# Optimization experiments

Hardware: AMD Instinct MI355X
Metric: run time of the kernel (lower is better)

Reference implementation:

```python
import jax, jax.numpy as jnp
import numpy as np

DECAY = 0.7      # membrane decay
THETA = 1.0      # spike threshold
K_WINNERS = 5
GAIN_UP = 1.5
GAIN_DOWN = 0.6

SEQ_LEN = 8192
VOCAB = 128000


def setup_inputs() -> dict:
    key = jax.random.key(0)
    token_seq = jax.random.randint(key, (SEQ_LEN,), 0, VOCAB)  # int token ids
    v0 = jnp.zeros((VOCAB,), jnp.float32)  # initial membrane potentials
    return {"token_seq": token_seq, "v0": v0, "vocab_size": VOCAB}


def reference(token_seq, v0, vocab_size):
    spikes0 = jnp.zeros((vocab_size,), jnp.float32)

    def lif_step(state, token_id):
        v, spikes = state
        t = jnp.clip(token_id, 0, vocab_size - 1).astype(jnp.int32)
        v_new = DECAY * v[t] + 1.0                      # gather + decay + input current
        spiked = v_new >= THETA
        v = v.at[t].set(jnp.where(spiked, v_new - THETA, v_new))  # reset-by-subtraction
        spikes = spikes.at[t].add(spiked.astype(jnp.float32))
        return (v, spikes), None

    (v_final, spikes_final), _ = jax.lax.scan(lif_step, (v0, spikes0), token_seq)

    k = min(K_WINNERS, int(vocab_size))
    _, top_idx = jax.lax.top_k(v_final, k)
    winners = jnp.zeros((vocab_size,), jnp.float32).at[top_idx].set(1.0)
    gains = jnp.where(winners > 0, GAIN_UP,
                      jnp.where(spikes_final > 0, GAIN_DOWN, 1.0))
    return gains
```

## Files before the change

### kernel.cpp

```cpp
#include <hip/hip_runtime.h>
#include <float.h>
#include <limits.h>

#define DECAY 0.7f
#define THETA 1.0f
#define KWIN 5
#define GAIN_UP 1.5f
#define GAIN_DOWN 0.6f

#define NT 256
#define SLICE 1024

__device__ __forceinline__ void lif_replay(float v0, int n, float& v_out, int& spikes_out) {
    float v = v0;
    int s = 0;
    for (int i = 0; i < n; ++i) {
        float vn = __fadd_rn(__fmul_rn(DECAY, v), 1.0f);
        if (vn >= THETA) { v = __fsub_rn(vn, THETA); ++s; }
        else             { v = vn; }
    }
    v_out = v;
    spikes_out = s;
}

__device__ __forceinline__ void better(float& bv, int& bi, float ov, int oi) {
    if (ov > bv || (ov == bv && oi < bi)) { bv = ov; bi = oi; }
}

__global__ void fused_local(const int* __restrict__ tok,
                            const float* __restrict__ v0,
                            int n, int vocab,
                            float* __restrict__ out,
                            float* __restrict__ cand_v,
                            int* __restrict__ cand_i) {
    __shared__ int hist[SLICE];

    const int tid  = threadIdx.x;
    const int bid  = blockIdx.x;
    const int wave = tid >> 6;
    const int lane = tid & 63;
    const int sbase = bid * SLICE;

    #pragma unroll
    for (int k = 0; k < SLICE / NT; ++k) {
        hist[k * NT + tid] = 0;
    }
    __syncthreads();

    int nv4 = n & ~3;
    for (int j = tid * 4; j < nv4; j += NT * 4) {
        int4 t4 = *(const int4*)(tok + j);
        int t; unsigned r;
        t = min(max(t4.x, 0), vocab - 1); r = (unsigned)(t - sbase); if (r < SLICE) atomicAdd(&hist[r], 1);
        t = min(max(t4.y, 0), vocab - 1); r = (unsigned)(t - sbase); if (r < SLICE) atomicAdd(&hist[r], 1);
        t = min(max(t4.z, 0), vocab - 1); r = (unsigned)(t - sbase); if (r < SLICE) atomicAdd(&hist[r], 1);
        t = min(max(t4.w, 0), vocab - 1); r = (unsigned)(t - sbase); if (r < SLICE) atomicAdd(&hist[r], 1);
    }
    for (int j = nv4 + tid; j < n; j += NT) {
        int t = min(max(tok[j], 0), vocab - 1);
        unsigned r = (unsigned)(t - sbase);
        if (r < SLICE) atomicAdd(&hist[r], 1);
    }
    __syncthreads();

    const int wbase = wave * 256;
    float lv[4];
    int   li[4];
    #pragma unroll
    for (int k = 0; k < 4; ++k) {
        int off = wbase + k * 64 + lane;
        int idx = sbase + off;
        float vf = -FLT_MAX;
        int   id = -1;
        if (idx < vocab) {
            int c = hist[off];
            int s;
            lif_replay(v0[idx], c, vf, s);
            out[idx] = (s > 0) ? GAIN_DOWN : 1.0f;
            id = idx;
        }
        lv[k] = vf;
        li[k] = id;
    }

    const int gw = bid * (NT / 64) + wave;
    #pragma unroll
    for (int r = 0; r < KWIN; ++r) {
        float bv = -FLT_MAX;
        int   bi = INT_MAX;
        #pragma unroll
        for (int k = 0; k < 4; ++k) {
            if (li[k] >= 0) better(bv, bi, lv[k], li[k]);
        }
        #pragma unroll
        for (int off = 32; off > 0; off >>= 1) {
            float ov = __shfl_xor(bv, off, 64);
            int   oi = __shfl_xor(bi, off, 64);
            better(bv, bi, ov, oi);
        }
        if (lane == 0) {
            cand_v[gw * KWIN + r] = bv;
            cand_i[gw * KWIN + r] = bi;
        }
        #pragma unroll
        for (int k = 0; k < 4; ++k) {
            if (li[k] == bi) li[k] = -1;
        }
    }
}

#define MAXC 10

__global__ void merge_top5(const float* __restrict__ cand_v,
                           const int* __restrict__ cand_i,
                           int n_cand,
                           float* __restrict__ out) {
    __shared__ unsigned long long swk[4];

    const int tid  = threadIdx.x;
    const int wave = tid >> 6;
    const int lane = tid & 63;

    unsigned long long k0 = 0ULL, k1 = 0ULL, k2 = 0ULL, k3 = 0ULL, k4 = 0ULL;
    unsigned long long k5 = 0ULL, k6 = 0ULL, k7 = 0ULL, k8 = 0ULL, k9 = 0ULL;
    #pragma unroll
    for (int s = 0; s < MAXC; ++s) {
        int j = s * 256 + tid;
        unsigned long long key = 0ULL;
        if (j < n_cand) {
            int ci = cand_i[j];
            if (ci >= 0 && ci != INT_MAX) {
                unsigned b  = __float_as_uint(cand_v[j]);
                unsigned sv = (b & 0x80000000u) ? ~b : (b | 0x80000000u);
                key = ((unsigned long long)sv << 32) | (unsigned)(~(unsigned)ci);
            }
        }
        if (s == 0) k0 = key; else if (s == 1) k1 = key;
        else if (s == 2) k2 = key; else if (s == 3) k3 = key;
        else if (s == 4) k4 = key; else if (s == 5) k5 = key;
        else if (s == 6) k6 = key; else if (s == 7) k7 = key;
        else if (s == 8) k8 = key; else k9 = key;
    }

    unsigned long long thresh = ~0ULL;
    for (int r = 0; r < KWIN; ++r) {
        unsigned long long best = 0ULL;
        if (k0 < thresh && k0 > best) best = k0;
        if (k1 < thresh && k1 > best) best = k1;
        if (k2 < thresh && k2 > best) best = k2;
        if (k3 < thresh && k3 > best) best = k3;
        if (k4 < thresh && k4 > best) best = k4;
        if (k5 < thresh && k5 > best) best = k5;
        if (k6 < thresh && k6 > best) best = k6;
        if (k7 < thresh && k7 > best) best = k7;
        if (k8 < thresh && k8 > best) best = k8;
        if (k9 < thresh && k9 > best) best = k9;

        #pragma unroll
        for (int off = 32; off > 0; off >>= 1) {
            unsigned hi = (unsigned)(best >> 32);
            unsigned lo = (unsigned)(best & 0xFFFFFFFFu);
            unsigned ohi = __shfl_xor(hi, off, 64);
            unsigned olo = __shfl_xor(lo, off, 64);
            unsigned long long ok = ((unsigned long long)ohi << 32) | olo;
            if (ok > best) best = ok;
        }
        if (lane == 0) swk[wave] = best;
        __syncthreads();

        unsigned long long bb = swk[0];
        if (swk[1] > bb) bb = swk[1];
        if (swk[2] > bb) bb = swk[2];
        if (swk[3] > bb) bb = swk[3];
        __syncthreads();

        if (tid == 0 && bb != 0ULL) {
            unsigned inv = (unsigned)(bb & 0xFFFFFFFFu);
            int idx = (int)(~inv);
            out[idx] = GAIN_UP;
        }
        thresh = bb;
    }
}

extern "C" void kernel_launch(void* const* d_in, const int* in_sizes, int n_in,
                              void* d_out, int out_size, void* d_ws, size_t ws_size,
                              hipStream_t stream) {
    const int*   tok = (const int*)d_in[0];
    const float* v0  = (const float*)d_in[1];
    int n     = in_sizes[0];
    int vocab = in_sizes[1];
    float* out = (float*)d_out;

    int nb     = (vocab + SLICE - 1) / SLICE;
    int nwaves = nb * (NT / 64);

    float* cand_v = (float*)d_ws;
    int*   cand_i = (int*)(cand_v + (size_t)nwaves * KWIN);

    fused_local<<<nb, NT, 0, stream>>>(tok, v0, n, vocab, out, cand_v, cand_i);
    merge_top5<<<1, NT, 0, stream>>>(cand_v, cand_i, nwaves * KWIN, out);
}
```

Baseline: 74.78 us.

## Merge into single kernel with per-block full hash histogram and global top-5

```diff
diff --git a/kernel.cpp b/kernel.cpp
--- a/kernel.cpp
+++ b/kernel.cpp
@@ -8,8 +8,15 @@
 #define GAIN_UP 1.5f
 #define GAIN_DOWN 0.6f
 
-#define NT 256
+#define NT 1024
+#define NWAVES (NT / 64)
 #define SLICE 1024
+#define NSLOT 16384
+#define HMASK (NSLOT - 1)
+#define HEMPTY 0xFFFFFFFFu
+#define CBITS 14
+#define CMASK ((1u << CBITS) - 1u)
+#define BWORDS 4096
 
 __device__ __forceinline__ void lif_replay(float v0, int n, float& v_out, int& spikes_out) {
     float v = v0;
@@ -23,143 +30,125 @@
     spikes_out = s;
 }
 
-__device__ __forceinline__ void better(float& bv, int& bi, float ov, int oi) {
-    if (ov > bv || (ov == bv && oi < bi)) { bv = ov; bi = oi; }
+__device__ __forceinline__ unsigned long long mkkey(float v, int idx) {
+    unsigned b  = __float_as_uint(v);
+    unsigned sv = (b & 0x80000000u) ? ~b : (b | 0x80000000u);
+    return ((unsigned long long)sv << 32) | (unsigned)(~(unsigned)idx);
 }
 
-__global__ void fused_local(const int* __restrict__ tok,
-                            const float* __restrict__ v0,
-                            int n, int vocab,
-                            float* __restrict__ out,
-                            float* __restrict__ cand_v,
-                            int* __restrict__ cand_i) {
-    __shared__ int hist[SLICE];
+__global__ __launch_bounds__(NT) void fused_one(const int* __restrict__ tok,
+                                                const float* __restrict__ v0,
+                                                int n, int vocab,
+                                                float* __restrict__ out) {
+    __shared__ unsigned hsl[NSLOT];
+    __shared__ unsigned bmap[BWORDS];
+    __shared__ unsigned long long swk[NWAVES];
 
-    const int tid  = threadIdx.x;
-    const int bid  = blockIdx.x;
-    const int wave = tid >> 6;
-    const int lane = tid & 63;
+    const int tid   = threadIdx.x;
+    const int bid   = blockIdx.x;
+    const int wave  = tid >> 6;
+    const int lane  = tid & 63;
     const int sbase = bid * SLICE;
 
     #pragma unroll
-    for (int k = 0; k < SLICE / NT; ++k) {
-        hist[k * NT + tid] = 0;
-    }
+    for (int k = 0; k < NSLOT / NT; ++k) hsl[k * NT + tid] = HEMPTY;
+    #pragma unroll
+    for (int k = 0; k < BWORDS / NT; ++k) bmap[k * NT + tid] = 0u;
     __syncthreads();
 
+    auto insert_tok = [&](int traw) {
+        int t = min(max(traw, 0), vocab - 1);
+        atomicOr(&bmap[t >> 5], 1u << (t & 31));
+        unsigned h = ((unsigned)t * 2654435761u) >> 18;
+        for (;;) {
+            unsigned cur = hsl[h];
+            if (cur != HEMPTY && (cur >> CBITS) == (unsigned)t) { atomicAdd(&hsl[h], 1u); break; }
+            if (cur == HEMPTY) {
+                unsigned old = atomicCAS(&hsl[h], HEMPTY, ((unsigned)t << CBITS) | 1u);
+                if (old == HEMPTY) break;
+                if ((old >> CBITS) == (unsigned)t) { atomicAdd(&hsl[h], 1u); break; }
+            }
+            h = (h + 1) & HMASK;
+        }
+    };
     int nv4 = n & ~3;
     for (int j = tid * 4; j < nv4; j += NT * 4) {
         int4 t4 = *(const int4*)(tok + j);
-        int t; unsigned r;
-        t = min(max(t4.x, 0), vocab - 1); r = (unsigned)(t - sbase); if (r < SLICE) atomicAdd(&hist[r], 1);
-        t = min(max(t4.y, 0), vocab - 1); r = (unsigned)(t - sbase); if (r < SLICE) atomicAdd(&hist[r], 1);
-        t = min(max(t4.z, 0), vocab - 1); r = (unsigned)(t - sbase); if (r < SLICE) atomicAdd(&hist[r], 1);
-        t = min(max(t4.w, 0), vocab - 1); r = (unsigned)(t - sbase); if (r < SLICE) atomicAdd(&hist[r], 1);
+        insert_tok(t4.x); insert_tok(t4.y); insert_tok(t4.z); insert_tok(t4.w);
     }
-    for (int j = nv4 + tid; j < n; j += NT) {
-        int t = min(max(tok[j], 0), vocab - 1);
-        unsigned r = (unsigned)(t - sbase);
-        if (r < SLICE) atomicAdd(&hist[r], 1);
-    }
+    for (int j = nv4 + tid; j < n; j += NT) insert_tok(tok[j]);
     __syncthreads();
 
-    const int wbase = wave * 256;
-    float lv[4];
-    int   li[4];
-    #pragma unroll
-    for (int k = 0; k < 4; ++k) {
-        int off = wbase + k * 64 + lane;
-        int idx = sbase + off;
-        float vf = -FLT_MAX;
-        int   id = -1;
-        if (idx < vocab) {
-            int c = hist[off];
-            int s;
-            lif_replay(v0[idx], c, vf, s);
-            out[idx] = (s > 0) ? GAIN_DOWN : 1.0f;
-            id = idx;
+    auto lookup_cnt = [&](int idx) -> int {
+        unsigned h = ((unsigned)idx * 2654435761u) >> 18;
+        for (;;) {
+            unsigned cur = hsl[h];
+            if (cur == HEMPTY) return 0;
+            if ((cur >> CBITS) == (unsigned)idx) return (int)(cur & CMASK);
+            h = (h + 1) & HMASK;
         }
-        lv[k] = vf;
-        li[k] = id;
+    };
+
+    unsigned long long k0 = 0ULL, k1 = 0ULL, k2 = 0ULL, k3 = 0ULL, k4 = 0ULL;
+
+    auto consider = [&](float vf, int idx) {
+        unsigned long long key = mkkey(vf, idx);
+        if (key > k4) {
+            if      (key > k0) { k4 = k3; k3 = k2; k2 = k1; k1 = k0; k0 = key; }
+            else if (key > k1) { k4 = k3; k3 = k2; k2 = k1; k1 = key; }
+            else if (key > k2) { k4 = k3; k3 = k2; k2 = key; }
+            else if (key > k3) { k4 = k3; k3 = key; }
+            else               { k4 = key; }
+        }
+    };
+
+    for (int base = tid * 4; base < vocab; base += NT * 4) {
+        if (base + 3 < vocab) {
+            float4 v4 = *(const float4*)(v0 + base);
+            unsigned bw = bmap[base >> 5];
+            unsigned sh = (unsigned)(base & 31);
+            float g0, g1, g2, g3;
+            float vf; int s;
+
+            if ((bw >> (sh + 0)) & 1u) { lif_replay(v4.x, lookup_cnt(base + 0), vf, s); } else { vf = v4.x; s = 0; }
+            g0 = (s > 0) ? GAIN_DOWN : 1.0f; consider(vf, base + 0);
+            if ((bw >> (sh + 1)) & 1u) { lif_replay(v4.y, lookup_cnt(base + 1), vf, s); } else { vf = v4.y; s = 0; }
+            g1 = (s > 0) ? GAIN_DOWN : 1.0f; consider(vf, base + 1);
+            if ((bw >> (sh + 2)) & 1u) { lif_replay(v4.z, lookup_cnt(base + 2), vf, s); } else { vf = v4.z; s = 0; }
+            g2 = (s > 0) ? GAIN_DOWN : 1.0f; consider(vf, base + 2);
+            if ((bw >> (sh + 3)) & 1u) { lif_replay(v4.w, lookup_cnt(base + 3), vf, s); } else { vf = v4.w; s = 0; }
+            g3 = (s > 0) ? GAIN_DOWN : 1.0f; consider(vf, base + 3);
+
+            if ((unsigned)(base - sbase) < SLICE) {
+                *(float4*)(out + base) = make_float4(g0, g1, g2, g3);
+            }
+        } else {
+            for (int idx = base; idx < vocab; ++idx) {
+                float v = v0[idx];
+                float vf; int s;
+                if ((bmap[idx >> 5] >> (idx & 31)) & 1u) { lif_replay(v, lookup_cnt(idx), vf, s); }
+                else { vf = v; s = 0; }
+                if ((unsigned)(idx - sbase) < SLICE) out[idx] = (s > 0) ? GAIN_DOWN : 1.0f;
+                consider(vf, idx);
+            }
+        }
     }
 
-    const int gw = bid * (NT / 64) + wave;
-    #pragma unroll
-    for (int r = 0; r < KWIN; ++r) {
-        float bv = -FLT_MAX;
-        int   bi = INT_MAX;
-        #pragma unroll
-        for (int k = 0; k < 4; ++k) {
-            if (li[k] >= 0) better(bv, bi, lv[k], li[k]);
-        }
-        #pragma unroll
-        for (int off = 32; off > 0; off >>= 1) {
-            float ov = __shfl_xor(bv, off, 64);
-            int   oi = __shfl_xor(bi, off, 64);
-            better(bv, bi, ov, oi);
-        }
-        if (lane == 0) {
-            cand_v[gw * KWIN + r] = bv;
-            cand_i[gw * KWIN + r] = bi;
-        }
-        #pragma unroll
-        for (int k = 0; k < 4; ++k) {
-            if (li[k] == bi) li[k] = -1;
-        }
-    }
-}
-
-#define MAXC 10
-
-__global__ void merge_top5(const float* __restrict__ cand_v,
-                           const int* __restrict__ cand_i,
-                           int n_cand,
-                           float* __restrict__ out) {
-    __shared__ unsigned long long swk[4];
-
-    const int tid  = threadIdx.x;
-    const int wave = tid >> 6;
-    const int lane = tid & 63;
-
-    unsigned long long k0 = 0ULL, k1 = 0ULL, k2 = 0ULL, k3 = 0ULL, k4 = 0ULL;
-    unsigned long long k5 = 0ULL, k6 = 0ULL, k7 = 0ULL, k8 = 0ULL, k9 = 0ULL;
-    #pragma unroll
-    for (int s = 0; s < MAXC; ++s) {
-        int j = s * 256 + tid;
-        unsigned long long key = 0ULL;
-        if (j < n_cand) {
-            int ci = cand_i[j];
-            if (ci >= 0 && ci != INT_MAX) {
-                unsigned b  = __float_as_uint(cand_v[j]);
-                unsigned sv = (b & 0x80000000u) ? ~b : (b | 0x80000000u);
-                key = ((unsigned long long)sv << 32) | (unsigned)(~(unsigned)ci);
-            }
-        }
-        if (s == 0) k0 = key; else if (s == 1) k1 = key;
-        else if (s == 2) k2 = key; else if (s == 3) k3 = key;
-        else if (s == 4) k4 = key; else if (s == 5) k5 = key;
-        else if (s == 6) k6 = key; else if (s == 7) k7 = key;
-        else if (s == 8) k8 = key; else k9 = key;
-    }
+    __syncthreads();
 
     unsigned long long thresh = ~0ULL;
     for (int r = 0; r < KWIN; ++r) {
-        unsigned long long best = 0ULL;
-        if (k0 < thresh && k0 > best) best = k0;
-        if (k1 < thresh && k1 > best) best = k1;
-        if (k2 < thresh && k2 > best) best = k2;
-        if (k3 < thresh && k3 > best) best = k3;
-        if (k4 < thresh && k4 > best) best = k4;
-        if (k5 < thresh && k5 > best) best = k5;
-        if (k6 < thresh && k6 > best) best = k6;
-        if (k7 < thresh && k7 > best) best = k7;
-        if (k8 < thresh && k8 > best) best = k8;
-        if (k9 < thresh && k9 > best) best = k9;
+        unsigned long long best =
+            (k0 < thresh) ? k0 :
+            (k1 < thresh) ? k1 :
+            (k2 < thresh) ? k2 :
+            (k3 < thresh) ? k3 :
+            (k4 < thresh) ? k4 : 0ULL;
 
         #pragma unroll
         for (int off = 32; off > 0; off >>= 1) {
-            unsigned hi = (unsigned)(best >> 32);
-            unsigned lo = (unsigned)(best & 0xFFFFFFFFu);
+            unsigned hi  = (unsigned)(best >> 32);
+            unsigned lo  = (unsigned)(best & 0xFFFFFFFFu);
             unsigned ohi = __shfl_xor(hi, off, 64);
             unsigned olo = __shfl_xor(lo, off, 64);
             unsigned long long ok = ((unsigned long long)ohi << 32) | olo;
@@ -169,15 +158,15 @@
         __syncthreads();
 
         unsigned long long bb = swk[0];
-        if (swk[1] > bb) bb = swk[1];
-        if (swk[2] > bb) bb = swk[2];
-        if (swk[3] > bb) bb = swk[3];
+        #pragma unroll
+        for (int w = 1; w < NWAVES; ++w) {
+            if (swk[w] > bb) bb = swk[w];
+        }
         __syncthreads();
 
         if (tid == 0 && bb != 0ULL) {
-            unsigned inv = (unsigned)(bb & 0xFFFFFFFFu);
-            int idx = (int)(~inv);
-            out[idx] = GAIN_UP;
+            int idx = (int)(~(unsigned)(bb & 0xFFFFFFFFu));
+            if ((unsigned)(idx - sbase) < SLICE) out[idx] = GAIN_UP;
         }
         thresh = bb;
     }
@@ -192,12 +181,6 @@
     int vocab = in_sizes[1];
     float* out = (float*)d_out;
 
-    int nb     = (vocab + SLICE - 1) / SLICE;
-    int nwaves = nb * (NT / 64);
-
-    float* cand_v = (float*)d_ws;
-    int*   cand_i = (int*)(cand_v + (size_t)nwaves * KWIN);
-
-    fused_local<<<nb, NT, 0, stream>>>(tok, v0, n, vocab, out, cand_v, cand_i);
-    merge_top5<<<1, NT, 0, stream>>>(cand_v, cand_i, nwaves * KWIN, out);
+    int nb = (vocab + SLICE - 1) / SLICE;
+    fused_one<<<nb, NT, 0, stream>>>(tok, v0, n, vocab, out);
 }
```

Result: slower. 160.8 us (+115.1%).
